# Performance work log

Measured on AMD Instinct MI355X. Metric: run time of the kernel, lower is better.

## Reference

```python
import jax, jax.numpy as jnp
import numpy as np

N, C, H, W, HD = 32, 24, 12, 12, 128
GT, FP, A = 256, 256, 28
DIN = (C + 2) * 2 + HD  # 180, g_theta input dim


def setup_inputs() -> dict:
    key = jax.random.key(0)
    ks = jax.random.split(key, 18)
    def w(k, shape):
        fan_in = shape[0]
        return jax.random.normal(k, shape, jnp.float32) / np.sqrt(fan_in).astype(np.float32)
    inp = {
        "x": jax.random.normal(ks[0], (N, C, H, W), jnp.float32),
        "q": jax.random.normal(ks[1], (N, HD), jnp.float32),
        "gW0": w(ks[2], (DIN, GT)), "gb0": jnp.zeros((GT,), jnp.float32),
        "gW1": w(ks[3], (GT, GT)),  "gb1": jnp.zeros((GT,), jnp.float32),
        "gW2": w(ks[4], (GT, GT)),  "gb2": jnp.zeros((GT,), jnp.float32),
        "gW3": w(ks[5], (GT, GT)),  "gb3": jnp.zeros((GT,), jnp.float32),
        "fW0": w(ks[6], (GT, FP)),  "fb0": jnp.zeros((FP,), jnp.float32),
        "fW1": w(ks[7], (FP, FP)),  "fb1": jnp.zeros((FP,), jnp.float32),
        "fW2": w(ks[8], (FP, A)),   "fb2": jnp.zeros((A,), jnp.float32),
    }
    return inp


def _rn_forward(x, q, gW0, gb0, gW1, gb1, gW2, gb2, gW3, gb3,
                fW0, fb0, fW1, fb1, fW2, fb2):
    n, c, h, w = x.shape
    o = h * w
    # rn_encode: per-object features + (x, y) coordinates in [-1, 1]
    feats = x.reshape(n, c, o).transpose(0, 2, 1)            # [n, o, c]
    xc = jnp.repeat(jnp.linspace(-1.0, 1.0, h), w)           # row coord per pixel
    yc = jnp.tile(jnp.linspace(-1.0, 1.0, w), h)             # col coord per pixel
    coords = jnp.stack([xc, yc], axis=-1).astype(x.dtype)    # [o, 2]
    feats = jnp.concatenate([feats, jnp.broadcast_to(coords, (n, o, 2))], axis=-1)  # [n, o, c+2]
    cp = c + 2
    # pairs[n, a, b] = [feats[b], feats[a], q]  (matches torch unsqueeze(1)/unsqueeze(2))
    pairs = jnp.concatenate([
        jnp.broadcast_to(feats[:, None, :, :], (n, o, o, cp)),
        jnp.broadcast_to(feats[:, :, None, :], (n, o, o, cp)),
        jnp.broadcast_to(q[:, None, None, :], (n, o, o, q.shape[1])),
    ], axis=-1)                                              # [n, o, o, 2*cp+hd]
    # g_theta: 4-layer ReLU MLP applied per pair
    hdd = pairs
    for Wm, b in ((gW0, gb0), (gW1, gb1), (gW2, gb2), (gW3, gb3)):
        hdd = jax.nn.relu(jnp.einsum('nabd,de->nabe', hdd, Wm) + b)
    # lower_sum: keep lower-triangular (incl. diagonal) pairs, sum over them
    mask = jnp.tril(jnp.ones((o, o), hdd.dtype))[None, :, :, None]
    rel = jnp.sum(hdd * mask, axis=(1, 2))                   # [n, GT]
    # f_phi: ReLU hidden layers, linear output (dropout = eval mode no-op)
    y = jax.nn.relu(rel @ fW0 + fb0)
    y = jax.nn.relu(y @ fW1 + fb1)
    logits = y @ fW2 + fb2                                   # [n, A]
    return logits


def reference(x, q, gW0, gb0, gW1, gb1, gW2, gb2, gW3, gb3,
              fW0, fb0, fW1, fb1, fW2, fb2):
    return _rn_forward(x, q, gW0, gb0, gW1, gb1, gW2, gb2, gW3, gb3,
                       fW0, fb0, fW1, fb1, fW2, fb2)
```

## Files before the change

### kernel.cpp

```cpp
#include <hip/hip_runtime.h>
#include <hip/hip_bf16.h>

typedef __attribute__((ext_vector_type(8))) short short8;
typedef __attribute__((ext_vector_type(4))) float f32x4;

#define O 144
#define NB 32
#define GT 256
#define NPAIRS 10440
#define TP 96
#define NT 109
#define GRID (NB*NT)
#define CHUNK 436

#define WS_WT   0u
#define WS_U    393216u
#define WS_V    2752512u
#define WS_REL  5144576u
#define WS_CNT  5177344u

__device__ __forceinline__ unsigned short f2bf(float f){
  unsigned int uu = __builtin_bit_cast(unsigned int, f);
  unsigned int lsb = (uu >> 16) & 1u;
  uu += 0x7fffu + lsb;
  return (unsigned short)(uu >> 16);
}
__device__ __forceinline__ unsigned int cvtpk(float lo, float hi){
  unsigned int r;
  asm("v_cvt_pk_bf16_f32 %0, %1, %2" : "=v"(r) : "v"(lo), "v"(hi));
  return r;
}

__global__ void prep_all(const float* __restrict__ x, const float* __restrict__ q,
                         const float* __restrict__ gW0, const float* __restrict__ gb0,
                         const float* __restrict__ gW1, const float* __restrict__ gW2,
                         const float* __restrict__ gW3,
                         unsigned short* __restrict__ u, unsigned short* __restrict__ v,
                         unsigned short* __restrict__ WtP, float* __restrict__ rel,
                         int* __restrict__ cnt){
  int blk = blockIdx.x, t = threadIdx.x;
  if (blk < 256){
    __shared__ float xs[24][18];
    __shared__ float qs[128];
    int n = blk >> 3, oq = blk & 7;
    int o0 = oq * 18;
    for (int i = t; i < 432; i += 256){
      int c = i / 18, oo = i - c*18;
      xs[c][oo] = x[(n*24 + c)*144 + o0 + oo];
    }
    if (t < 128) qs[t] = q[n*128 + t];
    __syncthreads();
    float wq = gb0[t];
    for (int d = 0; d < 128; d++) wq += qs[d] * gW0[(52 + d)*GT + t];
    float wc[52];
    #pragma unroll
    for (int c = 0; c < 52; c++) wc[c] = gW0[c*GT + t];
    for (int oo = 0; oo < 18; oo++){
      int o = o0 + oo;
      float xc = -1.f + 2.f * (float)(o / 12) / 11.f;
      float yc = -1.f + 2.f * (float)(o % 12) / 11.f;
      float su = wq + xc*wc[24] + yc*wc[25];
      float sv =      xc*wc[50] + yc*wc[51];
      #pragma unroll
      for (int c = 0; c < 24; c++){ float f = xs[c][oo]; su += f*wc[c]; sv += f*wc[26+c]; }
      u[(size_t)(n*O + o)*GT + t] = f2bf(su);
      v[(size_t)(n*O + o)*GT + t] = f2bf(sv);
    }
  } else {
    int b2 = blk - 256;
    int li = b2 >> 8, e = b2 & 255;
    int k = t;
    const float* W = (li == 0) ? gW1 : (li == 1) ? gW2 : gW3;
    int et = e >> 4, r = e & 15;
    int kk = k >> 5, g = (k >> 3) & 3, d = k & 7;
    WtP[li*65536 + et*4096 + kk*512 + r*32 + g*8 + d] = f2bf(W[k*GT + e]);
    if (b2 < NB) rel[b2*GT + t] = 0.f;
    if (b2 == 0 && t < NB) cnt[t] = 0;
  }
}

__global__ __launch_bounds__(256, 2) void rn_main(
    const unsigned short* __restrict__ u, const unsigned short* __restrict__ v,
    const unsigned short* __restrict__ WtP,
    const float* __restrict__ gb1, const float* __restrict__ gb2,
    const float* __restrict__ gb3, float* __restrict__ rel, int* __restrict__ cnt,
    const float* __restrict__ fW0, const float* __restrict__ fb0,
    const float* __restrict__ fW1, const float* __restrict__ fb1,
    const float* __restrict__ fW2, const float* __restrict__ fb2,
    float* __restrict__ out)
{
  __shared__ short8 hbuf[3072];
  char* lds = (char*)hbuf;

  const int tid  = threadIdx.x;
  const int lane = tid & 63;
  const int wav  = tid >> 6;
  int lg = (blockIdx.x & 7)*CHUNK + (blockIdx.x >> 3);
  const int n    = lg / NT;
  const int tile = lg - n*NT;
  const int tbase = tile * TP;
  const int l15 = lane & 15, l4 = lane >> 4;

  const unsigned short* wb = WtP + wav*16384 + l15*32 + l4*8;
  short8 aA0,aA1,aA2,aA3, aB0,aB1,aB2,aB3, aC0,aC1,aC2,aC3;
#define LA(s0,s1,s2,s3,p_) { const unsigned short* _wp = wb + ((p_) >> 3)*65536 + ((p_) & 7)*512; \
    s0 = *(const short8*)(_wp);        s1 = *(const short8*)(_wp + 4096); \
    s2 = *(const short8*)(_wp + 8192); s3 = *(const short8*)(_wp + 12288); }
  LA(aA0,aA1,aA2,aA3, 0)
  LA(aB0,aB1,aB2,aB3, 1)
  LA(aC0,aC1,aC2,aC3, 2)

  if (tid < 192){
    int row = tid >> 1;
    int pt  = tbase + row;
    bool valid = pt < NPAIRS;
    int pa = 0, pb = 0;
    if (valid){
      pa = (int)((sqrtf(8.f*(float)pt + 1.f) - 1.f) * 0.5f);
      while ((pa + 1)*(pa + 2)/2 <= pt) pa++;
      while (pa*(pa + 1)/2 > pt) pa--;
      pb = pt - pa*(pa + 1)/2;
    }
    const uint4* up4 = (const uint4*)(u + (size_t)(n*O + pb)*GT);
    const uint4* vp4 = (const uint4*)(v + (size_t)(n*O + pa)*GT);
    int half = tid & 1;
    int sbase = row*512 + half*256;
    int ts = (row & 7) << 4;
    #pragma unroll
    for (int cc = 0; cc < 16; cc++){
      uint4 hv;
      if (valid){
        uint4 uu = up4[half*16 + cc];
        uint4 vv = vp4[half*16 + cc];
        #pragma unroll
        for (int j = 0; j < 4; j++){
          unsigned int ud = (&uu.x)[j], vd = (&vv.x)[j];
          float lo = __builtin_bit_cast(float, ud << 16) + __builtin_bit_cast(float, vd << 16);
          float hi = __builtin_bit_cast(float, ud & 0xffff0000u) + __builtin_bit_cast(float, vd & 0xffff0000u);
          (&hv.x)[j] = cvtpk(fmaxf(lo, 0.f), fmaxf(hi, 0.f));
        }
      } else {
        hv = (uint4){0u, 0u, 0u, 0u};
      }
      *(uint4*)(lds + sbase + ((cc*16) ^ ts)) = hv;
    }
  }
  __syncthreads();

  const bool fullvalid = (tbase + TP <= NPAIRS);
  const int swz01 = (l15 & 3) << 4;
  const int swz2  = (l15 & 4) << 4;
  const int rbE = l15*512 + ((l4*16) ^ swz01) + swz2;
  const int rbO = l15*512 + ((l4*16) ^ swz01) - swz2;
  const int ebase = l15*512 + wav*128 + ((l4*8) ^ ((l15 & 1) << 4)) + ((l15 & 6) << 4);
  f32x4 acc[4][6];

#define MFMA16(s0,s1,s2,s3,kk_) { \
    const int rb_ = ((kk_) & 1) ? rbO : rbE; \
    short8 b_[6]; \
    _Pragma("unroll") \
    for (int jp = 0; jp < 6; jp++) b_[jp] = *(short8*)(lds + rb_ + jp*8192 + (kk_)*64); \
    __builtin_amdgcn_s_setprio(1); \
    _Pragma("unroll") \
    for (int jp = 0; jp < 6; jp++){ \
      acc[0][jp] = __builtin_amdgcn_mfma_f32_16x16x32_bf16(s0, b_[jp], acc[0][jp], 0, 0, 0); \
      acc[1][jp] = __builtin_amdgcn_mfma_f32_16x16x32_bf16(s1, b_[jp], acc[1][jp], 0, 0, 0); \
      acc[2][jp] = __builtin_amdgcn_mfma_f32_16x16x32_bf16(s2, b_[jp], acc[2][jp], 0, 0, 0); \
      acc[3][jp] = __builtin_amdgcn_mfma_f32_16x16x32_bf16(s3, b_[jp], acc[3][jp], 0, 0, 0); } \
    __builtin_amdgcn_s_setprio(0); }

  #pragma unroll
  for (int L = 0; L < 3; L++){
    const float* gb = (L == 0) ? gb1 : (L == 1) ? gb2 : gb3;

    #pragma unroll
    for (int ie = 0; ie < 4; ie++){
      f32x4 bbv = *(const f32x4*)(gb + wav*64 + ie*16 + l4*4);
      #pragma unroll
      for (int jp = 0; jp < 6; jp++) acc[ie][jp] = bbv;
    }

    #pragma unroll
    for (int kk = 0; kk < 8; kk++){
      const int p = L*8 + kk;
      const int pn = (p + 3 > 23) ? 23 : p + 3;
      if ((p % 3) == 0)      { MFMA16(aA0,aA1,aA2,aA3,kk) LA(aA0,aA1,aA2,aA3,pn) }
      else if ((p % 3) == 1) { MFMA16(aB0,aB1,aB2,aB3,kk) LA(aB0,aB1,aB2,aB3,pn) }
      else                   { MFMA16(aC0,aC1,aC2,aC3,kk) LA(aC0,aC1,aC2,aC3,pn) }
    }

    if (L < 2){
      __syncthreads();
      #pragma unroll
      for (int ie = 0; ie < 4; ie++){
        int ea = ebase ^ (ie*32);
        #pragma unroll
        for (int jp = 0; jp < 6; jp++){
          uint2 pk;
          pk.x = cvtpk(fmaxf(acc[ie][jp][0], 0.f), fmaxf(acc[ie][jp][1], 0.f));
          pk.y = cvtpk(fmaxf(acc[ie][jp][2], 0.f), fmaxf(acc[ie][jp][3], 0.f));
          *(uint2*)(lds + ea + jp*8192) = pk;
        }
      }
      __syncthreads();
    } else {
      #pragma unroll
      for (int ie = 0; ie < 4; ie++){
        int e0 = wav*64 + ie*16 + l4*4;
        f32x4 s = {0.f, 0.f, 0.f, 0.f};
        #pragma unroll
        for (int jp = 0; jp < 6; jp++){
          bool pv = fullvalid || (tbase + jp*16 + l15 < NPAIRS);
          #pragma unroll
          for (int j = 0; j < 4; j++){
            float hvv = fmaxf(acc[ie][jp][j], 0.f);
            s[j] += pv ? hvv : 0.f;
          }
        }
        #pragma unroll
        for (int st = 1; st < 16; st <<= 1){
          #pragma unroll
          for (int j = 0; j < 4; j++)
            s[j] += __shfl_xor(s[j], st);
        }
        if (l15 == 0){
          #pragma unroll
          for (int j = 0; j < 4; j++)
            atomicAdd(&rel[n*GT + e0 + j], s[j]);
        }
      }
    }
  }
#undef LA
#undef MFMA16

  __syncthreads();
  if (tid == 0) ((int*)lds)[0] = atomicAdd(&cnt[n], 1);
  __syncthreads();
  int done = ((int*)lds)[0];
  __syncthreads();
  if (done == NT - 1){
    float rv = atomicAdd(&rel[n*GT + tid], 0.f);
    float* hsm = (float*)lds;
    float* ysm = hsm + 256;
    int t = tid;
    hsm[t] = rv;
    __syncthreads();
    float s = fb0[t];
    for (int k = 0; k < 256; k++) s += hsm[k] * fW0[k*GT + t];
    ysm[t] = fmaxf(s, 0.f);
    __syncthreads();
    s = fb1[t];
    for (int k = 0; k < 256; k++) s += ysm[k] * fW1[k*GT + t];
    __syncthreads();
    hsm[t] = fmaxf(s, 0.f);
    __syncthreads();
    if (t < 28){
      s = fb2[t];
      for (int k = 0; k < 256; k++) s += hsm[k] * fW2[k*28 + t];
      out[n*28 + t] = s;
    }
  }
}

extern "C" void kernel_launch(void* const* d_in, const int* in_sizes, int n_in,
                              void* d_out, int out_size, void* d_ws, size_t ws_size,
                              hipStream_t stream){
  (void)in_sizes; (void)n_in; (void)out_size; (void)ws_size;
  const float* x   = (const float*)d_in[0];
  const float* q   = (const float*)d_in[1];
  const float* gW0 = (const float*)d_in[2];
  const float* gb0 = (const float*)d_in[3];
  const float* gW1 = (const float*)d_in[4];
  const float* gb1 = (const float*)d_in[5];
  const float* gW2 = (const float*)d_in[6];
  const float* gb2 = (const float*)d_in[7];
  const float* gW3 = (const float*)d_in[8];
  const float* gb3 = (const float*)d_in[9];
  const float* fW0 = (const float*)d_in[10];
  const float* fb0 = (const float*)d_in[11];
  const float* fW1 = (const float*)d_in[12];
  const float* fb1 = (const float*)d_in[13];
  const float* fW2 = (const float*)d_in[14];
  const float* fb2 = (const float*)d_in[15];

  char* ws = (char*)d_ws;
  unsigned short* WtP = (unsigned short*)(ws + WS_WT);
  unsigned short* u   = (unsigned short*)(ws + WS_U);
  unsigned short* v   = (unsigned short*)(ws + WS_V);
  float* rel = (float*)(ws + WS_REL);
  int*   cnt = (int*)(ws + WS_CNT);
  float* out = (float*)d_out;

  hipLaunchKernelGGL(prep_all, dim3(1024), dim3(256), 0, stream,
                     x, q, gW0, gb0, gW1, gW2, gW3, u, v, WtP, rel, cnt);
  hipLaunchKernelGGL(rn_main, dim3(GRID), dim3(256), 0, stream,
                     u, v, WtP, gb1, gb2, gb3, rel, cnt,
                     fW0, fb0, fW1, fb1, fW2, fb2, out);
}
```

Baseline: 241.7 us.

## Enlarge pair tile to 128 and double-buffer LDS B-fragment loads

Raises the pairs per block from 96 to 128, which cuts the tile count per batch and gives each wave 8 column fragments per MFMA sweep for more weight reuse. LDS B operands are now prefetched one k-step ahead into two alternating register buffers. The weight A-operand prefetch drops from three register sets to two to make room, and all 256 threads now take part in building the pair tile. The cost is higher register pressure (32 accumulators plus 16 B fragments) that may break the 2-blocks-per-CU launch bound or cause spills, plus larger LDS use and fewer blocks in the grid.

```diff
diff --git a/kernel.cpp b/kernel.cpp
--- a/kernel.cpp
+++ b/kernel.cpp
@@ -8,10 +8,10 @@
 #define NB 32
 #define GT 256
 #define NPAIRS 10440
-#define TP 96
-#define NT 109
+#define TP 128
+#define NT 82
 #define GRID (NB*NT)
-#define CHUNK 436
+#define CHUNK 328
 
 #define WS_WT   0u
 #define WS_U    393216u
@@ -89,7 +89,7 @@
     const float* __restrict__ fW2, const float* __restrict__ fb2,
     float* __restrict__ out)
 {
-  __shared__ short8 hbuf[3072];
+  __shared__ short8 hbuf[4096];
   char* lds = (char*)hbuf;
 
   const int tid  = threadIdx.x;
@@ -102,16 +102,15 @@
   const int l15 = lane & 15, l4 = lane >> 4;
 
   const unsigned short* wb = WtP + wav*16384 + l15*32 + l4*8;
-  short8 aA0,aA1,aA2,aA3, aB0,aB1,aB2,aB3, aC0,aC1,aC2,aC3;
+  short8 aP0,aP1,aP2,aP3, aQ0,aQ1,aQ2,aQ3;
 #define LA(s0,s1,s2,s3,p_) { const unsigned short* _wp = wb + ((p_) >> 3)*65536 + ((p_) & 7)*512; \
     s0 = *(const short8*)(_wp);        s1 = *(const short8*)(_wp + 4096); \
     s2 = *(const short8*)(_wp + 8192); s3 = *(const short8*)(_wp + 12288); }
-  LA(aA0,aA1,aA2,aA3, 0)
-  LA(aB0,aB1,aB2,aB3, 1)
-  LA(aC0,aC1,aC2,aC3, 2)
-
-  if (tid < 192){
-    int row = tid >> 1;
+  LA(aP0,aP1,aP2,aP3, 0)
+  LA(aQ0,aQ1,aQ2,aQ3, 1)
+
+  {
+    int row = wav*32 + (lane >> 1);
     int pt  = tbase + row;
     bool valid = pt < NPAIRS;
     int pa = 0, pb = 0;
@@ -123,9 +122,9 @@
     }
     const uint4* up4 = (const uint4*)(u + (size_t)(n*O + pb)*GT);
     const uint4* vp4 = (const uint4*)(v + (size_t)(n*O + pa)*GT);
-    int half = tid & 1;
+    int half = lane & 1;
     int sbase = row*512 + half*256;
-    int ts = (row & 7) << 4;
+    int ts = ((lane >> 1) & 7) << 4;
     #pragma unroll
     for (int cc = 0; cc < 16; cc++){
       uint4 hv;
@@ -153,20 +152,21 @@
   const int rbE = l15*512 + ((l4*16) ^ swz01) + swz2;
   const int rbO = l15*512 + ((l4*16) ^ swz01) - swz2;
   const int ebase = l15*512 + wav*128 + ((l4*8) ^ ((l15 & 1) << 4)) + ((l15 & 6) << 4);
-  f32x4 acc[4][6];
-
-#define MFMA16(s0,s1,s2,s3,kk_) { \
-    const int rb_ = ((kk_) & 1) ? rbO : rbE; \
-    short8 b_[6]; \
+  f32x4 acc[4][8];
+  short8 b0[8], b1[8];
+
+#define LOADB(dst_, kk_) { const int rb_ = ((kk_) & 1) ? rbO : rbE; \
     _Pragma("unroll") \
-    for (int jp = 0; jp < 6; jp++) b_[jp] = *(short8*)(lds + rb_ + jp*8192 + (kk_)*64); \
+    for (int jp = 0; jp < 8; jp++) dst_[jp] = *(short8*)(lds + rb_ + jp*8192 + (kk_)*64); }
+
+#define MFMAB(bb_, s0,s1,s2,s3) { \
     __builtin_amdgcn_s_setprio(1); \
     _Pragma("unroll") \
-    for (int jp = 0; jp < 6; jp++){ \
-      acc[0][jp] = __builtin_amdgcn_mfma_f32_16x16x32_bf16(s0, b_[jp], acc[0][jp], 0, 0, 0); \
-      acc[1][jp] = __builtin_amdgcn_mfma_f32_16x16x32_bf16(s1, b_[jp], acc[1][jp], 0, 0, 0); \
-      acc[2][jp] = __builtin_amdgcn_mfma_f32_16x16x32_bf16(s2, b_[jp], acc[2][jp], 0, 0, 0); \
-      acc[3][jp] = __builtin_amdgcn_mfma_f32_16x16x32_bf16(s3, b_[jp], acc[3][jp], 0, 0, 0); } \
+    for (int jp = 0; jp < 8; jp++){ \
+      acc[0][jp] = __builtin_amdgcn_mfma_f32_16x16x32_bf16(s0, bb_[jp], acc[0][jp], 0, 0, 0); \
+      acc[1][jp] = __builtin_amdgcn_mfma_f32_16x16x32_bf16(s1, bb_[jp], acc[1][jp], 0, 0, 0); \
+      acc[2][jp] = __builtin_amdgcn_mfma_f32_16x16x32_bf16(s2, bb_[jp], acc[2][jp], 0, 0, 0); \
+      acc[3][jp] = __builtin_amdgcn_mfma_f32_16x16x32_bf16(s3, bb_[jp], acc[3][jp], 0, 0, 0); } \
     __builtin_amdgcn_s_setprio(0); }
 
   #pragma unroll
@@ -177,16 +177,20 @@
     for (int ie = 0; ie < 4; ie++){
       f32x4 bbv = *(const f32x4*)(gb + wav*64 + ie*16 + l4*4);
       #pragma unroll
-      for (int jp = 0; jp < 6; jp++) acc[ie][jp] = bbv;
-    }
-
+      for (int jp = 0; jp < 8; jp++) acc[ie][jp] = bbv;
+    }
+
+    LOADB(b0, 0);
     #pragma unroll
     for (int kk = 0; kk < 8; kk++){
-      const int p = L*8 + kk;
-      const int pn = (p + 3 > 23) ? 23 : p + 3;
-      if ((p % 3) == 0)      { MFMA16(aA0,aA1,aA2,aA3,kk) LA(aA0,aA1,aA2,aA3,pn) }
-      else if ((p % 3) == 1) { MFMA16(aB0,aB1,aB2,aB3,kk) LA(aB0,aB1,aB2,aB3,pn) }
-      else                   { MFMA16(aC0,aC1,aC2,aC3,kk) LA(aC0,aC1,aC2,aC3,pn) }
+      const int p  = L*8 + kk;
+      const int pn = (p + 2 > 23) ? 23 : p + 2;
+      short8 c0,c1,c2,c3;
+      if (p & 1){ c0=aQ0; c1=aQ1; c2=aQ2; c3=aQ3; }
+      else      { c0=aP0; c1=aP1; c2=aP2; c3=aP3; }
+      if (kk < 7){ if (kk & 1) { LOADB(b0, kk + 1) } else { LOADB(b1, kk + 1) } }
+      if (p & 1){ LA(aQ0,aQ1,aQ2,aQ3, pn) } else { LA(aP0,aP1,aP2,aP3, pn) }
+      if (kk & 1){ MFMAB(b1, c0,c1,c2,c3) } else { MFMAB(b0, c0,c1,c2,c3) }
     }
 
     if (L < 2){
@@ -195,7 +199,7 @@
       for (int ie = 0; ie < 4; ie++){
         int ea = ebase ^ (ie*32);
         #pragma unroll
-        for (int jp = 0; jp < 6; jp++){
+        for (int jp = 0; jp < 8; jp++){
           uint2 pk;
           pk.x = cvtpk(fmaxf(acc[ie][jp][0], 0.f), fmaxf(acc[ie][jp][1], 0.f));
           pk.y = cvtpk(fmaxf(acc[ie][jp][2], 0.f), fmaxf(acc[ie][jp][3], 0.f));
@@ -209,7 +213,7 @@
         int e0 = wav*64 + ie*16 + l4*4;
         f32x4 s = {0.f, 0.f, 0.f, 0.f};
         #pragma unroll
-        for (int jp = 0; jp < 6; jp++){
+        for (int jp = 0; jp < 8; jp++){
           bool pv = fullvalid || (tbase + jp*16 + l15 < NPAIRS);
           #pragma unroll
           for (int j = 0; j < 4; j++){
@@ -232,7 +236,8 @@
     }
   }
 #undef LA
-#undef MFMA16
+#undef LOADB
+#undef MFMAB
 
   __syncthreads();
   if (tid == 0) ((int*)lds)[0] = atomicAdd(&cnt[n], 1);
```

Measured after the change: 260.5 us. +7.8%, slower.

## Shrink weight prefetch to one stage and raise occupancy to three blocks per CU

Applied to the files above, without the earlier changes.

Replaces the three-deep register ring of prefetched weight fragments with a single-stage prefetch (load the next k-slice while computing the current one), freeing registers. The launch bounds are raised from 2 to 3 blocks per CU to use those registers for more resident waves and better latency hiding. The prep kernel's q projection loop also gets an unroll pragma. The trade-off is a shorter prefetch distance for global weight loads, so each MFMA step depends on a load issued only one step earlier, plus a tighter register budget that could cause spills. LDS use of 48KB per block also has to allow three blocks per CU.

```diff
diff --git a/kernel.cpp b/kernel.cpp
--- a/kernel.cpp
+++ b/kernel.cpp
@@ -51,6 +51,7 @@
     if (t < 128) qs[t] = q[n*128 + t];
     __syncthreads();
     float wq = gb0[t];
+    #pragma unroll 8
     for (int d = 0; d < 128; d++) wq += qs[d] * gW0[(52 + d)*GT + t];
     float wc[52];
     #pragma unroll
@@ -79,7 +80,7 @@
   }
 }
 
-__global__ __launch_bounds__(256, 2) void rn_main(
+__global__ __launch_bounds__(256, 3) void rn_main(
     const unsigned short* __restrict__ u, const unsigned short* __restrict__ v,
     const unsigned short* __restrict__ WtP,
     const float* __restrict__ gb1, const float* __restrict__ gb2,
@@ -102,15 +103,13 @@
   const int l15 = lane & 15, l4 = lane >> 4;
 
   const unsigned short* wb = WtP + wav*16384 + l15*32 + l4*8;
-  short8 aA0,aA1,aA2,aA3, aB0,aB1,aB2,aB3, aC0,aC1,aC2,aC3;
-#define LA(s0,s1,s2,s3,p_) { const unsigned short* _wp = wb + ((p_) >> 3)*65536 + ((p_) & 7)*512; \
-    s0 = *(const short8*)(_wp);        s1 = *(const short8*)(_wp + 4096); \
-    s2 = *(const short8*)(_wp + 8192); s3 = *(const short8*)(_wp + 12288); }
-  LA(aA0,aA1,aA2,aA3, 0)
-  LA(aB0,aB1,aB2,aB3, 1)
-  LA(aC0,aC1,aC2,aC3, 2)
-
-  if (tid < 192){
+  short8 an0, an1, an2, an3;
+#define LOADA(p_) { const unsigned short* _wp = wb + ((p_) >> 3)*65536 + ((p_) & 7)*512; \
+    an0 = *(const short8*)(_wp);        an1 = *(const short8*)(_wp + 4096); \
+    an2 = *(const short8*)(_wp + 8192); an3 = *(const short8*)(_wp + 12288); }
+  LOADA(0);
+
+  if (tid < 2*TP){
     int row = tid >> 1;
     int pt  = tbase + row;
     bool valid = pt < NPAIRS;
@@ -155,20 +154,6 @@
   const int ebase = l15*512 + wav*128 + ((l4*8) ^ ((l15 & 1) << 4)) + ((l15 & 6) << 4);
   f32x4 acc[4][6];
 
-#define MFMA16(s0,s1,s2,s3,kk_) { \
-    const int rb_ = ((kk_) & 1) ? rbO : rbE; \
-    short8 b_[6]; \
-    _Pragma("unroll") \
-    for (int jp = 0; jp < 6; jp++) b_[jp] = *(short8*)(lds + rb_ + jp*8192 + (kk_)*64); \
-    __builtin_amdgcn_s_setprio(1); \
-    _Pragma("unroll") \
-    for (int jp = 0; jp < 6; jp++){ \
-      acc[0][jp] = __builtin_amdgcn_mfma_f32_16x16x32_bf16(s0, b_[jp], acc[0][jp], 0, 0, 0); \
-      acc[1][jp] = __builtin_amdgcn_mfma_f32_16x16x32_bf16(s1, b_[jp], acc[1][jp], 0, 0, 0); \
-      acc[2][jp] = __builtin_amdgcn_mfma_f32_16x16x32_bf16(s2, b_[jp], acc[2][jp], 0, 0, 0); \
-      acc[3][jp] = __builtin_amdgcn_mfma_f32_16x16x32_bf16(s3, b_[jp], acc[3][jp], 0, 0, 0); } \
-    __builtin_amdgcn_s_setprio(0); }
-
   #pragma unroll
   for (int L = 0; L < 3; L++){
     const float* gb = (L == 0) ? gb1 : (L == 1) ? gb2 : gb3;
@@ -182,11 +167,24 @@
 
     #pragma unroll
     for (int kk = 0; kk < 8; kk++){
+      short8 a0 = an0, a1 = an1, a2 = an2, a3 = an3;
       const int p = L*8 + kk;
-      const int pn = (p + 3 > 23) ? 23 : p + 3;
-      if ((p % 3) == 0)      { MFMA16(aA0,aA1,aA2,aA3,kk) LA(aA0,aA1,aA2,aA3,pn) }
-      else if ((p % 3) == 1) { MFMA16(aB0,aB1,aB2,aB3,kk) LA(aB0,aB1,aB2,aB3,pn) }
-      else                   { MFMA16(aC0,aC1,aC2,aC3,kk) LA(aC0,aC1,aC2,aC3,pn) }
+      const int pn = (p + 1 > 23) ? 23 : p + 1;
+      LOADA(pn);
+      const int rb = (kk & 1) ? rbO : rbE;
+      short8 b[6];
+      #pragma unroll
+      for (int jp = 0; jp < 6; jp++)
+        b[jp] = *(short8*)(lds + rb + jp*8192 + kk*64);
+      __builtin_amdgcn_s_setprio(1);
+      #pragma unroll
+      for (int jp = 0; jp < 6; jp++){
+        acc[0][jp] = __builtin_amdgcn_mfma_f32_16x16x32_bf16(a0, b[jp], acc[0][jp], 0, 0, 0);
+        acc[1][jp] = __builtin_amdgcn_mfma_f32_16x16x32_bf16(a1, b[jp], acc[1][jp], 0, 0, 0);
+        acc[2][jp] = __builtin_amdgcn_mfma_f32_16x16x32_bf16(a2, b[jp], acc[2][jp], 0, 0, 0);
+        acc[3][jp] = __builtin_amdgcn_mfma_f32_16x16x32_bf16(a3, b[jp], acc[3][jp], 0, 0, 0);
+      }
+      __builtin_amdgcn_s_setprio(0);
     }
 
     if (L < 2){
@@ -231,8 +229,7 @@
       }
     }
   }
-#undef LA
-#undef MFMA16
+#undef LOADA
 
   __syncthreads();
   if (tid == 0) ((int*)lds)[0] = atomicAdd(&cnt[n], 1);
```

Result: slower. 275.9 us (+14.2%).
